# Kernel tuning notes

Measured on AMD Instinct MI355X. Metric: run time of the kernel, lower is better.

Reference implementation:

```python
import jax, jax.numpy as jnp
import numpy as np

DIM = 512
HEADS = 8
DIM_HEAD = 64
BLOCK_SIZE = 2048
B, N = 4, 2048
EPS = 1e-5


def setup_inputs() -> dict:
    key = jax.random.key(0)
    ks = jax.random.split(key, 8)
    hd = HEADS * DIM_HEAD
    std = 0.02
    return {
        "x": jax.random.normal(ks[0], (B, N, DIM), dtype=jnp.float32),
        "ln_w": jnp.ones((DIM,), jnp.float32),
        "ln_b": jnp.zeros((DIM,), jnp.float32),
        # linear weights stored [in, out]
        "wq": jax.random.normal(ks[1], (DIM, hd), jnp.float32) * std,
        "wk": jax.random.normal(ks[2], (DIM, hd), jnp.float32) * std,
        "wv": jax.random.normal(ks[3], (DIM, hd), jnp.float32) * std,
        "bv": jnp.zeros((hd,), jnp.float32),
        "wo": jax.random.normal(ks[4], (hd, DIM), jnp.float32) * std,
        "bo": jnp.zeros((DIM,), jnp.float32),
        "pe": jax.random.normal(ks[5], (1, BLOCK_SIZE, DIM), jnp.float32) * std,
    }


def reference(x, ln_w, ln_b, wq, wk, wv, bv, wo, bo, pe):
    # x: [b, n, dim] (channel_last=True path)
    b, n, _ = x.shape
    x_in = x
    # LayerNorm over last dim
    mu = jnp.mean(x, axis=-1, keepdims=True)
    var = jnp.var(x, axis=-1, keepdims=True)
    h = (x - mu) * jax.lax.rsqrt(var + EPS) * ln_w + ln_b
    # positional embedding
    h = h + pe[:, :n]
    # QKV projections -> [b, heads, n, dim_head]
    def split_heads(t):
        return t.reshape(b, n, HEADS, DIM_HEAD).transpose(0, 2, 1, 3)
    q = split_heads(h @ wq)
    k = split_heads(h @ wk)
    v = split_heads(h @ wv + bv)
    # attention
    scale = float(DIM_HEAD) ** -0.5
    attn = jnp.einsum('bhid,bhjd->bhij', q, k) * scale
    attn = jax.nn.softmax(attn, axis=-1)
    out = jnp.einsum('bhij,bhjd->bhid', attn, v)
    out = out.transpose(0, 2, 1, 3).reshape(b, n, HEADS * DIM_HEAD)
    out = out @ wo + bo
    return x_in + out
```

## Files before the change

kernel.cpp:

```cpp
#include <hip/hip_runtime.h>


typedef __bf16 bf16;
typedef __bf16 bf16x2 __attribute__((ext_vector_type(2)));
typedef __bf16 bf16x4 __attribute__((ext_vector_type(4)));
typedef __bf16 bf16x8 __attribute__((ext_vector_type(8)));
typedef float  f32x4  __attribute__((ext_vector_type(4)));

#define MFMA16(a, b, c) __builtin_amdgcn_mfma_f32_16x16x32_bf16((a), (b), (c), 0, 0, 0)

#if __has_builtin(__builtin_amdgcn_exp2f)
#define EXP2(x) __builtin_amdgcn_exp2f(x)
#else
#define EXP2(x) exp2f(x)
#endif

__device__ __forceinline__ void gload16(const void* g, void* l) {
  __builtin_amdgcn_global_load_lds(
      (const __attribute__((address_space(1))) unsigned int*)g,
      (__attribute__((address_space(3))) unsigned int*)l, 16, 0, 0);
}

__global__ void wtrans_kernel(const float* __restrict__ wq, const float* __restrict__ wk,
                              const float* __restrict__ wv, const float* __restrict__ wo,
                              bf16* __restrict__ wqkvT, bf16* __restrict__ woT) {
  __shared__ float tile[32][33];
  int z = blockIdx.z;
  const float* src = (z == 0) ? wq : (z == 1) ? wk : (z == 2) ? wv : wo;
  bf16* dst = (z < 3) ? (wqkvT + (size_t)z * 512 * 512) : woT;
  int bx = blockIdx.x, by = blockIdx.y;
  int tx = threadIdx.x, ty = threadIdx.y;
#pragma unroll
  for (int yy = 0; yy < 4; ++yy)
    tile[ty + 8 * yy][tx] = src[(size_t)(by * 32 + ty + 8 * yy) * 512 + bx * 32 + tx];
  __syncthreads();
#pragma unroll
  for (int yy = 0; yy < 4; ++yy)
    dst[(size_t)(bx * 32 + ty + 8 * yy) * 512 + by * 32 + tx] = (bf16)tile[tx][ty + 8 * yy];
}

__global__ __launch_bounds__(256) void ln_pe_kernel(const float* __restrict__ x,
                                                    const float* __restrict__ w,
                                                    const float* __restrict__ b,
                                                    const float* __restrict__ pe,
                                                    bf16* __restrict__ h) {
  int row = blockIdx.x;
  int tid = threadIdx.x;
  const float2 xv = *(const float2*)(x + (size_t)row * 512 + tid * 2);
  float s = xv.x + xv.y;
  float ss = xv.x * xv.x + xv.y * xv.y;
#pragma unroll
  for (int off = 32; off; off >>= 1) {
    s += __shfl_xor(s, off);
    ss += __shfl_xor(ss, off);
  }
  __shared__ float ps[4], pss[4];
  int wave = tid >> 6;
  if ((tid & 63) == 0) { ps[wave] = s; pss[wave] = ss; }
  __syncthreads();
  s = ps[0] + ps[1] + ps[2] + ps[3];
  ss = pss[0] + pss[1] + pss[2] + pss[3];
  float mu = s * (1.0f / 512.0f);
  float var = ss * (1.0f / 512.0f) - mu * mu;
  float rs = rsqrtf(var + 1e-5f);
  int n = row & 2047;
  float2 wv2 = *(const float2*)(w + tid * 2);
  float2 bv2 = *(const float2*)(b + tid * 2);
  float2 pv2 = *(const float2*)(pe + (size_t)n * 512 + tid * 2);
  bf16x2 o;
  o[0] = (bf16)((xv.x - mu) * rs * wv2.x + bv2.x + pv2.x);
  o[1] = (bf16)((xv.y - mu) * rs * wv2.y + bv2.y + pv2.y);
  *(bf16x2*)(h + (size_t)row * 512 + tid * 2) = o;
}

__device__ __forceinline__ void gemm_tile(const bf16* __restrict__ A,
                                          const bf16* __restrict__ Bt,
                                          f32x4 acc[4][4]) {
  __shared__ char lds[32768];
  const int tid = threadIdx.x, wave = tid >> 6, lane = tid & 63;
  const int wrow = wave >> 1, wcol = wave & 1;
  const int l15 = lane & 15, lg = lane >> 4;
  const char* Ab = (const char*)A + (size_t)blockIdx.x * 128 * 1024;
  const char* Bb = (const char*)Bt + (size_t)blockIdx.y * 128 * 1024;
  const int r0 = wave * 32 + (lane >> 2);
  const int cb = (lane & 3) * 16;
  const size_t so = (size_t)r0 * 1024 + cb;

  const f32x4 z = {0.f, 0.f, 0.f, 0.f};
#pragma unroll
  for (int mi = 0; mi < 4; ++mi)
#pragma unroll
    for (int ni = 0; ni < 4; ++ni) acc[mi][ni] = z;

  {
    char* nb = lds;
    gload16(Ab + so, nb + wave * 2048);
    gload16(Ab + so + 16 * 1024, nb + wave * 2048 + 1024);
    gload16(Bb + so, nb + 8192 + wave * 2048);
    gload16(Bb + so + 16 * 1024, nb + 8192 + wave * 2048 + 1024);
  }
  __syncthreads();

  for (int kt = 0; kt < 16; ++kt) {
    if (kt < 15) {
      char* nb = lds + ((kt + 1) & 1) * 16384;
      const char* As = Ab + so + (kt + 1) * 64;
      const char* Bs = Bb + so + (kt + 1) * 64;
      gload16(As, nb + wave * 2048);
      gload16(As + 16 * 1024, nb + wave * 2048 + 1024);
      gload16(Bs, nb + 8192 + wave * 2048);
      gload16(Bs + 16 * 1024, nb + 8192 + wave * 2048 + 1024);
    }
    char* lA = lds + (kt & 1) * 16384;
    char* lB = lA + 8192;
    bf16x8 av[4], bv[4];
#pragma unroll
    for (int mi = 0; mi < 4; ++mi)
      av[mi] = *(const bf16x8*)(lA + (wrow * 64 + mi * 16 + l15) * 64 + lg * 16);
#pragma unroll
    for (int ni = 0; ni < 4; ++ni)
      bv[ni] = *(const bf16x8*)(lB + (wcol * 64 + ni * 16 + l15) * 64 + lg * 16);
#pragma unroll
    for (int mi = 0; mi < 4; ++mi)
#pragma unroll
      for (int ni = 0; ni < 4; ++ni)
        acc[mi][ni] = MFMA16(av[mi], bv[ni], acc[mi][ni]);
    __syncthreads();
  }
}

__global__ __launch_bounds__(256, 3) void gemm_qkv_kernel(
    const bf16* __restrict__ h, const bf16* __restrict__ wqkvT,
    const float* __restrict__ bvec, bf16* __restrict__ qo, bf16* __restrict__ ko,
    bf16* __restrict__ vo) {
  f32x4 acc[4][4];
  gemm_tile(h, wqkvT, acc);
  const int tid = threadIdx.x, wave = tid >> 6, lane = tid & 63;
  const int wrow = wave >> 1, wcol = wave & 1;
  const int l15 = lane & 15, lg = lane >> 4;
  const int row0 = blockIdx.x * 128 + wrow * 64;
  const int col0 = blockIdx.y * 128 + wcol * 64;
#pragma unroll
  for (int mi = 0; mi < 4; ++mi) {
#pragma unroll
    for (int ni = 0; ni < 4; ++ni) {
      int c = col0 + ni * 16 + l15;
      int proj = c >> 9;
      int wc = c & 511;
      int head = wc >> 6, d = wc & 63;
      int rb = row0 + mi * 16 + lg * 4;
      int bb = rb >> 11, n = rb & 2047;
      if (proj == 2) {
        float bias = bvec[wc];
        bf16x4 pv;
#pragma unroll
        for (int reg = 0; reg < 4; ++reg) pv[reg] = (bf16)(acc[mi][ni][reg] + bias);
        *(bf16x4*)(vo + ((size_t)(bb * 8 + head) * 64 + d) * 2048 + n) = pv;
      } else if (proj == 0) {
#pragma unroll
        for (int reg = 0; reg < 4; ++reg)
          qo[((size_t)(bb * 8 + head) * 2048 + (n + reg)) * 64 + d] =
              (bf16)(acc[mi][ni][reg] * (0.125f * 1.44269504f));
      } else {
#pragma unroll
        for (int reg = 0; reg < 4; ++reg)
          ko[((size_t)(bb * 8 + head) * 2048 + (n + reg)) * 64 + d] =
              (bf16)acc[mi][ni][reg];
      }
    }
  }
}

__global__ __launch_bounds__(256, 2) void attn_kernel(const bf16* __restrict__ q,
                                                      const bf16* __restrict__ k,
                                                      const bf16* __restrict__ v,
                                                      bf16* __restrict__ ao) {
  __shared__ char lds[49152];
  const int tid = threadIdx.x, wave = tid >> 6, lane = tid & 63;
  const int l15 = lane & 15, lg = lane >> 4;
  const int swzr = (l15 & 7) << 4;

  const int bid = blockIdx.x;
  const int xcd = bid & 7, slot = bid >> 3;
  const int bh = xcd + 8 * (slot >> 4);
  const int qt = slot & 15;
  const int bb = bh >> 3, hh = bh & 7;

  const char* ksrc = (const char*)(k + (size_t)bh * 2048 * 64);
  const char* vsrc = (const char*)(v + (size_t)bh * 64 * 2048);
  const int r0 = wave * 16 + (lane >> 3);
  const int colb = (lane & 7) * 16;
  const size_t ko0 = (size_t)r0 * 128 + (colb ^ ((r0 & 7) << 4));
  const size_t vo0 = (size_t)r0 * 4096 + (colb ^ ((r0 & 7) << 4));
  char* Pw = lds + 32768 + wave * 4096;

  const bf16* qbase = q + ((size_t)bh * 2048 + qt * 128 + wave * 32) * 64;
  bf16x8 qf[2][2];
#pragma unroll
  for (int mi = 0; mi < 2; ++mi)
#pragma unroll
    for (int dk = 0; dk < 2; ++dk)
      qf[mi][dk] = *(const bf16x8*)(qbase + (mi * 16 + l15) * 64 + dk * 32 + lg * 8);

  const f32x4 z = {0.f, 0.f, 0.f, 0.f};
  f32x4 oacc[2][4];
  float mrun[2] = {-1e30f, -1e30f}, lrun[2] = {0.f, 0.f};
#pragma unroll
  for (int mi = 0; mi < 2; ++mi)
#pragma unroll
    for (int ds = 0; ds < 4; ++ds) oacc[mi][ds] = z;

  gload16(ksrc + ko0, lds + wave * 2048);
  gload16(ksrc + ko0 + 1024, lds + wave * 2048 + 1024);
  gload16(vsrc + vo0, lds + 8192 + wave * 2048);
  gload16(vsrc + vo0 + 8 * 4096, lds + 8192 + wave * 2048 + 1024);
  __syncthreads();

  for (int t = 0; t < 32; ++t) {
    if (t + 1 < 32) {
      char* nb = lds + ((t + 1) & 1) * 16384;
      const char* ks = ksrc + (size_t)(t + 1) * 8192 + ko0;
      const char* vs = vsrc + (size_t)(t + 1) * 128 + vo0;
      gload16(ks, nb + wave * 2048);
      gload16(ks + 1024, nb + wave * 2048 + 1024);
      gload16(vs, nb + 8192 + wave * 2048);
      gload16(vs + 8 * 4096, nb + 8192 + wave * 2048 + 1024);
    }
    char* Ksh = lds + (t & 1) * 16384;
    char* Vsh = Ksh + 8192;

    bf16x8 kf[4][2];
#pragma unroll
    for (int kt = 0; kt < 4; ++kt)
#pragma unroll
      for (int dk = 0; dk < 2; ++dk)
        kf[kt][dk] = *(const bf16x8*)(Ksh + (kt * 16 + l15) * 128 +
                                      ((dk * 64 + lg * 16) ^ swzr));
    f32x4 sacc[2][4];
#pragma unroll
    for (int mi = 0; mi < 2; ++mi)
#pragma unroll
      for (int kt = 0; kt < 4; ++kt) sacc[mi][kt] = z;
#pragma unroll
    for (int mi = 0; mi < 2; ++mi)
#pragma unroll
      for (int dk = 0; dk < 2; ++dk)
#pragma unroll
        for (int kt = 0; kt < 4; ++kt)
          sacc[mi][kt] = MFMA16(kf[kt][dk], qf[mi][dk], sacc[mi][kt]);

#pragma unroll
    for (int mi = 0; mi < 2; ++mi) {
      float mt = sacc[mi][0][0];
#pragma unroll
      for (int kt = 0; kt < 4; ++kt)
#pragma unroll
        for (int reg = 0; reg < 4; ++reg)
          if (kt || reg) mt = fmaxf(mt, sacc[mi][kt][reg]);
      mt = fmaxf(mt, __shfl_xor(mt, 16));
      mt = fmaxf(mt, __shfl_xor(mt, 32));
      float mn = fmaxf(mrun[mi], mt);
      float rs = 0.f;
      float p[4][4];
#pragma unroll
      for (int kt = 0; kt < 4; ++kt)
#pragma unroll
        for (int reg = 0; reg < 4; ++reg) {
          p[kt][reg] = EXP2(sacc[mi][kt][reg] - mn);
          rs += p[kt][reg];
        }
      rs += __shfl_xor(rs, 16);
      rs += __shfl_xor(rs, 32);
#pragma unroll
      for (int kt = 0; kt < 4; ++kt) {
        bf16x4 pv;
#pragma unroll
        for (int reg = 0; reg < 4; ++reg) pv[reg] = (bf16)p[kt][reg];
        *(bf16x4*)(Pw + (mi * 16 + l15) * 128 + ((kt * 32 + lg * 8) ^ swzr)) = pv;
      }
      if (__any(mt > mrun[mi])) {
        float sc = EXP2(mrun[mi] - mn);
        mrun[mi] = mn;
        lrun[mi] *= sc;
        float scr[4];
#pragma unroll
        for (int reg = 0; reg < 4; ++reg) scr[reg] = __shfl(sc, lg * 4 + reg);
#pragma unroll
        for (int ds = 0; ds < 4; ++ds)
#pragma unroll
          for (int reg = 0; reg < 4; ++reg) oacc[mi][ds][reg] *= scr[reg];
      }
      lrun[mi] += rs;
    }

#pragma unroll
    for (int ks = 0; ks < 2; ++ks) {
      bf16x8 vf[4];
#pragma unroll
      for (int ds = 0; ds < 4; ++ds)
        vf[ds] = *(const bf16x8*)(Vsh + (ds * 16 + l15) * 128 +
                                  ((ks * 64 + lg * 16) ^ swzr));
#pragma unroll
      for (int mi = 0; mi < 2; ++mi) {
        bf16x8 pf = *(const bf16x8*)(Pw + (mi * 16 + l15) * 128 +
                                     ((ks * 64 + lg * 16) ^ swzr));
#pragma unroll
        for (int ds = 0; ds < 4; ++ds)
          oacc[mi][ds] = MFMA16(pf, vf[ds], oacc[mi][ds]);
      }
    }
    __syncthreads();
  }

  const int qrow0 = qt * 128 + wave * 32;
#pragma unroll
  for (int mi = 0; mi < 2; ++mi) {
#if __has_builtin(__builtin_amdgcn_rcpf)
    float rin = __builtin_amdgcn_rcpf(lrun[mi]);
#else
    float rin = 1.0f / lrun[mi];
#endif
    float rr[4];
#pragma unroll
    for (int reg = 0; reg < 4; ++reg) rr[reg] = __shfl(rin, lg * 4 + reg);
#pragma unroll
    for (int ds = 0; ds < 4; ++ds)
#pragma unroll
      for (int reg = 0; reg < 4; ++reg) {
        int n = qrow0 + mi * 16 + lg * 4 + reg;
        ao[((size_t)bb * 2048 + n) * 512 + hh * 64 + ds * 16 + l15] =
            (bf16)(oacc[mi][ds][reg] * rr[reg]);
      }
  }
}

__global__ __launch_bounds__(256, 3) void gemm_out_kernel(
    const bf16* __restrict__ ao, const bf16* __restrict__ woT,
    const float* __restrict__ bo, const float* __restrict__ x,
    float* __restrict__ out) {
  f32x4 acc[4][4];
  gemm_tile(ao, woT, acc);
  const int tid = threadIdx.x, wave = tid >> 6, lane = tid & 63;
  const int wrow = wave >> 1, wcol = wave & 1;
  const int l15 = lane & 15, lg = lane >> 4;
  const int row0 = blockIdx.x * 128 + wrow * 64;
  const int col0 = blockIdx.y * 128 + wcol * 64;
#pragma unroll
  for (int mi = 0; mi < 4; ++mi) {
#pragma unroll
    for (int ni = 0; ni < 4; ++ni) {
      int c = col0 + ni * 16 + l15;
      float bias = bo[c];
#pragma unroll
      for (int reg = 0; reg < 4; ++reg) {
        int r = row0 + mi * 16 + lg * 4 + reg;
        size_t ofs = (size_t)r * 512 + c;
        out[ofs] = acc[mi][ni][reg] + bias + x[ofs];
      }
    }
  }
}

extern "C" void kernel_launch(void* const* d_in, const int* in_sizes, int n_in,
                              void* d_out, int out_size, void* d_ws, size_t ws_size,
                              hipStream_t stream) {
  const float* x   = (const float*)d_in[0];
  const float* lnw = (const float*)d_in[1];
  const float* lnb = (const float*)d_in[2];
  const float* wq  = (const float*)d_in[3];
  const float* wk  = (const float*)d_in[4];
  const float* wv  = (const float*)d_in[5];
  const float* bv  = (const float*)d_in[6];
  const float* wo  = (const float*)d_in[7];
  const float* bo  = (const float*)d_in[8];
  const float* pe  = (const float*)d_in[9];
  float* out = (float*)d_out;

  char* ws = (char*)d_ws;
  bf16* hbuf  = (bf16*)(ws);
  bf16* wqkvT = (bf16*)(ws + 8388608);
  bf16* woT   = (bf16*)(ws + 9961472);
  bf16* qb    = (bf16*)(ws + 10485760);
  bf16* kb    = (bf16*)(ws + 18874368);
  bf16* vb    = (bf16*)(ws + 27262976);
  bf16* aob   = hbuf;

  hipLaunchKernelGGL(wtrans_kernel, dim3(16, 16, 4), dim3(32, 8), 0, stream,
                     wq, wk, wv, wo, wqkvT, woT);
  hipLaunchKernelGGL(ln_pe_kernel, dim3(8192), dim3(256), 0, stream,
                     x, lnw, lnb, pe, hbuf);
  hipLaunchKernelGGL(gemm_qkv_kernel, dim3(64, 12), dim3(256), 0, stream,
                     hbuf, wqkvT, bv, qb, kb, vb);
  hipLaunchKernelGGL(attn_kernel, dim3(512), dim3(256), 0, stream,
                     qb, kb, vb, aob);
  hipLaunchKernelGGL(gemm_out_kernel, dim3(64, 4), dim3(256), 0, stream,
                     aob, woT, bo, x, out);
}
```

Baseline: 194.3 us.

## Halve attention query tile, add lazy rescale, set MFMA priority, vectorize LayerNorm

The attention kernel now handles 64 query rows per block (16 per wave) instead of 128, doubling the grid to 1024 blocks and raising the occupancy target to 4 blocks with less LDS per block. It also adds a lazy online-softmax rescale that only triggers when the running max grows by more than a threshold. s_setprio is raised around MFMA sections in both the GEMM and attention loops. LayerNorm processes one row per wave with float4 loads and no LDS reduction. The cost is that each block re-streams K/V for fewer query rows, so K/V traffic doubles.

```diff
diff --git a/kernel.cpp b/kernel.cpp
--- a/kernel.cpp
+++ b/kernel.cpp
@@ -44,33 +44,35 @@
                                                     const float* __restrict__ b,
                                                     const float* __restrict__ pe,
                                                     bf16* __restrict__ h) {
-  int row = blockIdx.x;
-  int tid = threadIdx.x;
-  const float2 xv = *(const float2*)(x + (size_t)row * 512 + tid * 2);
-  float s = xv.x + xv.y;
-  float ss = xv.x * xv.x + xv.y * xv.y;
-#pragma unroll
-  for (int off = 32; off; off >>= 1) {
+  const int row = blockIdx.x * 4 + (threadIdx.x >> 6);
+  const int lane = threadIdx.x & 63;
+  const float4* xr = (const float4*)(x + (size_t)row * 512) + lane * 2;
+  const float4 a = xr[0], c = xr[1];
+  float s = a.x + a.y + a.z + a.w + c.x + c.y + c.z + c.w;
+  float ss = a.x * a.x + a.y * a.y + a.z * a.z + a.w * a.w +
+             c.x * c.x + c.y * c.y + c.z * c.z + c.w * c.w;
+#pragma unroll
+  for (int off = 1; off <= 32; off <<= 1) {
     s += __shfl_xor(s, off);
     ss += __shfl_xor(ss, off);
   }
-  __shared__ float ps[4], pss[4];
-  int wave = tid >> 6;
-  if ((tid & 63) == 0) { ps[wave] = s; pss[wave] = ss; }
-  __syncthreads();
-  s = ps[0] + ps[1] + ps[2] + ps[3];
-  ss = pss[0] + pss[1] + pss[2] + pss[3];
-  float mu = s * (1.0f / 512.0f);
-  float var = ss * (1.0f / 512.0f) - mu * mu;
-  float rs = rsqrtf(var + 1e-5f);
-  int n = row & 2047;
-  float2 wv2 = *(const float2*)(w + tid * 2);
-  float2 bv2 = *(const float2*)(b + tid * 2);
-  float2 pv2 = *(const float2*)(pe + (size_t)n * 512 + tid * 2);
-  bf16x2 o;
-  o[0] = (bf16)((xv.x - mu) * rs * wv2.x + bv2.x + pv2.x);
-  o[1] = (bf16)((xv.y - mu) * rs * wv2.y + bv2.y + pv2.y);
-  *(bf16x2*)(h + (size_t)row * 512 + tid * 2) = o;
+  const float mu = s * (1.0f / 512.0f);
+  const float var = ss * (1.0f / 512.0f) - mu * mu;
+  const float rs = rsqrtf(var + 1e-5f);
+  const float4* wr = (const float4*)w + lane * 2;
+  const float4* br = (const float4*)b + lane * 2;
+  const float4* pr = (const float4*)(pe + (size_t)(row & 2047) * 512) + lane * 2;
+  const float4 w0 = wr[0], w1 = wr[1], b0 = br[0], b1 = br[1], p0 = pr[0], p1 = pr[1];
+  bf16x8 o;
+  o[0] = (bf16)((a.x - mu) * rs * w0.x + b0.x + p0.x);
+  o[1] = (bf16)((a.y - mu) * rs * w0.y + b0.y + p0.y);
+  o[2] = (bf16)((a.z - mu) * rs * w0.z + b0.z + p0.z);
+  o[3] = (bf16)((a.w - mu) * rs * w0.w + b0.w + p0.w);
+  o[4] = (bf16)((c.x - mu) * rs * w1.x + b1.x + p1.x);
+  o[5] = (bf16)((c.y - mu) * rs * w1.y + b1.y + p1.y);
+  o[6] = (bf16)((c.z - mu) * rs * w1.z + b1.z + p1.z);
+  o[7] = (bf16)((c.w - mu) * rs * w1.w + b1.w + p1.w);
+  *(bf16x8*)(h + (size_t)row * 512 + lane * 8) = o;
 }
 
 __device__ __forceinline__ void gemm_tile(const bf16* __restrict__ A,
@@ -120,11 +122,13 @@
 #pragma unroll
     for (int ni = 0; ni < 4; ++ni)
       bv[ni] = *(const bf16x8*)(lB + (wcol * 64 + ni * 16 + l15) * 64 + lg * 16);
+    __builtin_amdgcn_s_setprio(1);
 #pragma unroll
     for (int mi = 0; mi < 4; ++mi)
 #pragma unroll
       for (int ni = 0; ni < 4; ++ni)
         acc[mi][ni] = MFMA16(av[mi], bv[ni], acc[mi][ni]);
+    __builtin_amdgcn_s_setprio(0);
     __syncthreads();
   }
 }
@@ -171,19 +175,19 @@
   }
 }
 
-__global__ __launch_bounds__(256, 2) void attn_kernel(const bf16* __restrict__ q,
+__global__ __launch_bounds__(256, 4) void attn_kernel(const bf16* __restrict__ q,
                                                       const bf16* __restrict__ k,
                                                       const bf16* __restrict__ v,
                                                       bf16* __restrict__ ao) {
-  __shared__ char lds[49152];
+  __shared__ char lds[40960];
   const int tid = threadIdx.x, wave = tid >> 6, lane = tid & 63;
   const int l15 = lane & 15, lg = lane >> 4;
   const int swzr = (l15 & 7) << 4;
 
   const int bid = blockIdx.x;
   const int xcd = bid & 7, slot = bid >> 3;
-  const int bh = xcd + 8 * (slot >> 4);
-  const int qt = slot & 15;
+  const int bh = xcd + 8 * (slot >> 5);
+  const int qt = slot & 31;
   const int bb = bh >> 3, hh = bh & 7;
 
   const char* ksrc = (const char*)(k + (size_t)bh * 2048 * 64);
@@ -192,23 +196,17 @@
   const int colb = (lane & 7) * 16;
   const size_t ko0 = (size_t)r0 * 128 + (colb ^ ((r0 & 7) << 4));
   const size_t vo0 = (size_t)r0 * 4096 + (colb ^ ((r0 & 7) << 4));
-  char* Pw = lds + 32768 + wave * 4096;
-
-  const bf16* qbase = q + ((size_t)bh * 2048 + qt * 128 + wave * 32) * 64;
-  bf16x8 qf[2][2];
-#pragma unroll
-  for (int mi = 0; mi < 2; ++mi)
-#pragma unroll
-    for (int dk = 0; dk < 2; ++dk)
-      qf[mi][dk] = *(const bf16x8*)(qbase + (mi * 16 + l15) * 64 + dk * 32 + lg * 8);
+  char* Pw = lds + 32768 + wave * 2048;
+
+  const bf16* qbase = q + ((size_t)bh * 2048 + qt * 64 + wave * 16) * 64;
+  bf16x8 qf[2];
+#pragma unroll
+  for (int dk = 0; dk < 2; ++dk)
+    qf[dk] = *(const bf16x8*)(qbase + l15 * 64 + dk * 32 + lg * 8);
 
   const f32x4 z = {0.f, 0.f, 0.f, 0.f};
-  f32x4 oacc[2][4];
-  float mrun[2] = {-1e30f, -1e30f}, lrun[2] = {0.f, 0.f};
-#pragma unroll
-  for (int mi = 0; mi < 2; ++mi)
-#pragma unroll
-    for (int ds = 0; ds < 4; ++ds) oacc[mi][ds] = z;
+  f32x4 oacc[4] = {z, z, z, z};
+  float mrun = -1e30f, lrun = 0.f;
 
   gload16(ksrc + ko0, lds + wave * 2048);
   gload16(ksrc + ko0 + 1024, lds + wave * 2048 + 1024);
@@ -229,6 +227,7 @@
     char* Ksh = lds + (t & 1) * 16384;
     char* Vsh = Ksh + 8192;
 
+    __builtin_amdgcn_s_setprio(1);
     bf16x8 kf[4][2];
 #pragma unroll
     for (int kt = 0; kt < 4; ++kt)
@@ -236,102 +235,82 @@
       for (int dk = 0; dk < 2; ++dk)
         kf[kt][dk] = *(const bf16x8*)(Ksh + (kt * 16 + l15) * 128 +
                                       ((dk * 64 + lg * 16) ^ swzr));
-    f32x4 sacc[2][4];
-#pragma unroll
-    for (int mi = 0; mi < 2; ++mi)
-#pragma unroll
-      for (int kt = 0; kt < 4; ++kt) sacc[mi][kt] = z;
-#pragma unroll
-    for (int mi = 0; mi < 2; ++mi)
-#pragma unroll
-      for (int dk = 0; dk < 2; ++dk)
-#pragma unroll
-        for (int kt = 0; kt < 4; ++kt)
-          sacc[mi][kt] = MFMA16(kf[kt][dk], qf[mi][dk], sacc[mi][kt]);
-
-#pragma unroll
-    for (int mi = 0; mi < 2; ++mi) {
-      float mt = sacc[mi][0][0];
+    f32x4 sacc[4] = {z, z, z, z};
+#pragma unroll
+    for (int dk = 0; dk < 2; ++dk)
 #pragma unroll
       for (int kt = 0; kt < 4; ++kt)
-#pragma unroll
-        for (int reg = 0; reg < 4; ++reg)
-          if (kt || reg) mt = fmaxf(mt, sacc[mi][kt][reg]);
-      mt = fmaxf(mt, __shfl_xor(mt, 16));
-      mt = fmaxf(mt, __shfl_xor(mt, 32));
-      float mn = fmaxf(mrun[mi], mt);
-      float rs = 0.f;
-      float p[4][4];
-#pragma unroll
-      for (int kt = 0; kt < 4; ++kt)
-#pragma unroll
-        for (int reg = 0; reg < 4; ++reg) {
-          p[kt][reg] = EXP2(sacc[mi][kt][reg] - mn);
-          rs += p[kt][reg];
-        }
-      rs += __shfl_xor(rs, 16);
-      rs += __shfl_xor(rs, 32);
-#pragma unroll
-      for (int kt = 0; kt < 4; ++kt) {
-        bf16x4 pv;
-#pragma unroll
-        for (int reg = 0; reg < 4; ++reg) pv[reg] = (bf16)p[kt][reg];
-        *(bf16x4*)(Pw + (mi * 16 + l15) * 128 + ((kt * 32 + lg * 8) ^ swzr)) = pv;
+        sacc[kt] = MFMA16(kf[kt][dk], qf[dk], sacc[kt]);
+    __builtin_amdgcn_s_setprio(0);
+
+    float mt = fmaxf(fmaxf(sacc[0][0], sacc[0][1]), fmaxf(sacc[0][2], sacc[0][3]));
+#pragma unroll
+    for (int kt = 1; kt < 4; ++kt)
+      mt = fmaxf(mt, fmaxf(fmaxf(sacc[kt][0], sacc[kt][1]),
+                           fmaxf(sacc[kt][2], sacc[kt][3])));
+    mt = fmaxf(mt, __shfl_xor(mt, 16));
+    mt = fmaxf(mt, __shfl_xor(mt, 32));
+    if (__any(mt > mrun + 11.5f)) {
+      float mn = fmaxf(mrun, mt);
+      float sc = EXP2(mrun - mn);
+      mrun = mn;
+      lrun *= sc;
+      float scr[4];
+#pragma unroll
+      for (int reg = 0; reg < 4; ++reg) scr[reg] = __shfl(sc, lg * 4 + reg);
+#pragma unroll
+      for (int ds = 0; ds < 4; ++ds)
+#pragma unroll
+        for (int reg = 0; reg < 4; ++reg) oacc[ds][reg] *= scr[reg];
+    }
+    float rs = 0.f;
+#pragma unroll
+    for (int kt = 0; kt < 4; ++kt) {
+      bf16x4 pv;
+#pragma unroll
+      for (int reg = 0; reg < 4; ++reg) {
+        float p = EXP2(sacc[kt][reg] - mrun);
+        pv[reg] = (bf16)p;
+        rs += p;
       }
-      if (__any(mt > mrun[mi])) {
-        float sc = EXP2(mrun[mi] - mn);
-        mrun[mi] = mn;
-        lrun[mi] *= sc;
-        float scr[4];
-#pragma unroll
-        for (int reg = 0; reg < 4; ++reg) scr[reg] = __shfl(sc, lg * 4 + reg);
-#pragma unroll
-        for (int ds = 0; ds < 4; ++ds)
-#pragma unroll
-          for (int reg = 0; reg < 4; ++reg) oacc[mi][ds][reg] *= scr[reg];
+      *(bf16x4*)(Pw + l15 * 128 + ((kt * 32 + lg * 8) ^ swzr)) = pv;
+    }
+    rs += __shfl_xor(rs, 16);
+    rs += __shfl_xor(rs, 32);
+    lrun += rs;
+
+    __builtin_amdgcn_s_setprio(1);
+#pragma unroll
+    for (int ks = 0; ks < 2; ++ks) {
+      bf16x8 pf = *(const bf16x8*)(Pw + l15 * 128 + ((ks * 64 + lg * 16) ^ swzr));
+#pragma unroll
+      for (int ds = 0; ds < 4; ++ds) {
+        bf16x8 vf = *(const bf16x8*)(Vsh + (ds * 16 + l15) * 128 +
+                                     ((ks * 64 + lg * 16) ^ swzr));
+        oacc[ds] = MFMA16(pf, vf, oacc[ds]);
       }
-      lrun[mi] += rs;
-    }
-
-#pragma unroll
-    for (int ks = 0; ks < 2; ++ks) {
-      bf16x8 vf[4];
-#pragma unroll
-      for (int ds = 0; ds < 4; ++ds)
-        vf[ds] = *(const bf16x8*)(Vsh + (ds * 16 + l15) * 128 +
-                                  ((ks * 64 + lg * 16) ^ swzr));
-#pragma unroll
-      for (int mi = 0; mi < 2; ++mi) {
-        bf16x8 pf = *(const bf16x8*)(Pw + (mi * 16 + l15) * 128 +
-                                     ((ks * 64 + lg * 16) ^ swzr));
-#pragma unroll
-        for (int ds = 0; ds < 4; ++ds)
-          oacc[mi][ds] = MFMA16(pf, vf[ds], oacc[mi][ds]);
-      }
-    }
+    }
+    __builtin_amdgcn_s_setprio(0);
     __syncthreads();
   }
 
-  const int qrow0 = qt * 128 + wave * 32;
-#pragma unroll
-  for (int mi = 0; mi < 2; ++mi) {
+  const int qrow0 = qt * 64 + wave * 16;
 #if __has_builtin(__builtin_amdgcn_rcpf)
-    float rin = __builtin_amdgcn_rcpf(lrun[mi]);
+  float rin = __builtin_amdgcn_rcpf(lrun);
 #else
-    float rin = 1.0f / lrun[mi];
+  float rin = 1.0f / lrun;
 #endif
-    float rr[4];
-#pragma unroll
-    for (int reg = 0; reg < 4; ++reg) rr[reg] = __shfl(rin, lg * 4 + reg);
-#pragma unroll
-    for (int ds = 0; ds < 4; ++ds)
-#pragma unroll
-      for (int reg = 0; reg < 4; ++reg) {
-        int n = qrow0 + mi * 16 + lg * 4 + reg;
-        ao[((size_t)bb * 2048 + n) * 512 + hh * 64 + ds * 16 + l15] =
-            (bf16)(oacc[mi][ds][reg] * rr[reg]);
-      }
-  }
+  float rr[4];
+#pragma unroll
+  for (int reg = 0; reg < 4; ++reg) rr[reg] = __shfl(rin, lg * 4 + reg);
+#pragma unroll
+  for (int ds = 0; ds < 4; ++ds)
+#pragma unroll
+    for (int reg = 0; reg < 4; ++reg) {
+      int n = qrow0 + lg * 4 + reg;
+      ao[((size_t)bb * 2048 + n) * 512 + hh * 64 + ds * 16 + l15] =
+          (bf16)(oacc[ds][reg] * rr[reg]);
+    }
 }
 
 __global__ __launch_bounds__(256, 3) void gemm_out_kernel(
@@ -387,11 +366,11 @@
 
   hipLaunchKernelGGL(wtrans_kernel, dim3(16, 16, 4), dim3(32, 8), 0, stream,
                      wq, wk, wv, wo, wqkvT, woT);
-  hipLaunchKernelGGL(ln_pe_kernel, dim3(8192), dim3(256), 0, stream,
+  hipLaunchKernelGGL(ln_pe_kernel, dim3(2048), dim3(256), 0, stream,
                      x, lnw, lnb, pe, hbuf);
   hipLaunchKernelGGL(gemm_qkv_kernel, dim3(64, 12), dim3(256), 0, stream,
                      hbuf, wqkvT, bv, qb, kb, vb);
-  hipLaunchKernelGGL(attn_kernel, dim3(512), dim3(256), 0, stream,
+  hipLaunchKernelGGL(attn_kernel, dim3(1024), dim3(256), 0, stream,
                      qb, kb, vb, aob);
   hipLaunchKernelGGL(gemm_out_kernel, dim3(64, 4), dim3(256), 0, stream,
                      aob, woT, bo, x, out);
```

After: 179.5 us. 1.08x faster.
